# Kernel optimization log

Hardware: AMD Instinct MI355X
Metric: run time of the kernel (lower is better)

## Reference

```python
import jax, jax.numpy as jnp
import numpy as np

N_EMBED = 1024
HIDDEN = 2752  # find_multiple(int(8/3*1024), 32)
NUM_EXPERTS = 8
TOP_K = 2
AUX_COEFF = 0.01


def _swiglu(x, wg, wu, wd):
    # x: [N,C]; wg,wu: [H,C]; wd: [C,H]  (nn.Linear weight layout, y = x @ W.T)
    return (jax.nn.silu(x @ wg.T) * (x @ wu.T)) @ wd.T


def setup_inputs() -> dict:
    key = jax.random.key(0)
    ks = jax.random.split(key, 8)
    s = 0.02
    return {
        "x": jax.random.normal(ks[0], (2, 2048, N_EMBED), dtype=jnp.float32),
        "gate_w": jax.random.normal(ks[1], (NUM_EXPERTS, N_EMBED), dtype=jnp.float32) * s,
        "expert_gate_w": jax.random.normal(ks[2], (NUM_EXPERTS, HIDDEN, N_EMBED), dtype=jnp.float32) * s,
        "expert_up_w": jax.random.normal(ks[3], (NUM_EXPERTS, HIDDEN, N_EMBED), dtype=jnp.float32) * s,
        "expert_down_w": jax.random.normal(ks[4], (NUM_EXPERTS, N_EMBED, HIDDEN), dtype=jnp.float32) * s,
        "shared_gate_w": jax.random.normal(ks[5], (HIDDEN, N_EMBED), dtype=jnp.float32) * s,
        "shared_up_w": jax.random.normal(ks[6], (HIDDEN, N_EMBED), dtype=jnp.float32) * s,
        "shared_down_w": jax.random.normal(ks[7], (N_EMBED, HIDDEN), dtype=jnp.float32) * s,
    }


def reference(x, gate_w, expert_gate_w, expert_up_w, expert_down_w,
              shared_gate_w, shared_up_w, shared_down_w):
    B, T, C = x.shape
    xf = x.reshape(-1, C)                      # [N, C]
    N = xf.shape[0]

    # shared expert (always-on)
    shared_out = _swiglu(xf, shared_gate_w, shared_up_w, shared_down_w)

    # gating
    logits = xf @ gate_w.T                     # [N, E]
    top_w, top_i = jax.lax.top_k(logits, TOP_K)
    top_w = jax.nn.softmax(top_w.astype(jnp.float32), axis=-1)  # [N, K]

    # load-balancing aux loss
    mask = jax.nn.one_hot(top_i, NUM_EXPERTS, dtype=jnp.float32).sum(axis=1)  # [N, E]
    frac_selected = mask.mean(axis=0)
    mean_probs = jax.nn.softmax(logits.astype(jnp.float32), axis=-1).mean(axis=0)
    aux_loss = AUX_COEFF * (frac_selected * mean_probs).sum()

    # dense per-token per-expert combine weights (0 for unselected experts)
    w_dense = jnp.zeros((N, NUM_EXPERTS), jnp.float32)
    w_dense = w_dense.at[jnp.arange(N)[:, None], top_i].add(top_w)  # [N, E]

    routed = jnp.zeros_like(xf)
    for e in range(NUM_EXPERTS):
        routed = routed + _swiglu(xf, expert_gate_w[e], expert_up_w[e],
                                  expert_down_w[e]) * w_dense[:, e:e + 1]

    final = (shared_out + routed).reshape(B, T, C)
    return final, aux_loss
```

## Files before the change

### kernel.cpp

```cpp
#include <hip/hip_runtime.h>
#include <hip/hip_bf16.h>
#include <math.h>

#define N_TOK 4096
#define CDIM 1024
#define HDIM 2752
#define NEXP 8

typedef __bf16 bf16_t;
typedef __bf16 bf16x8 __attribute__((ext_vector_type(8)));
typedef float f32x4 __attribute__((ext_vector_type(4)));

__device__ __forceinline__ void gload_lds16(const void* g, void* l) {
  __builtin_amdgcn_global_load_lds(
      (const __attribute__((address_space(1))) unsigned int*)g,
      (__attribute__((address_space(3))) unsigned int*)l, 16, 0, 0);
}

__device__ __forceinline__ int xcd_swz(int orig, int nwg) {
  int q = nwg >> 3, r = nwg & 7;
  int xcd = orig & 7, lin = orig >> 3;
  return (xcd < r ? xcd * (q + 1) : r * (q + 1) + (xcd - r) * q) + lin;
}

struct CastG {
  const float* src[4];
  bf16_t* dst[4];
  int start[5];
  const float* x;
  const float* gw;
  int* top_i; float* top_w; float* probs_tok; bf16_t* xb;
};
__global__ void moe_cast_gate(CastG c) {
  const int b = blockIdx.x;
  if (b < c.start[4]) {
    int k = 0;
#pragma unroll
    for (int i = 0; i < 3; ++i) k += (b >= c.start[i + 1]);
    size_t i4 = (size_t)(b - c.start[k]) * 256 + threadIdx.x;
    float4 v = ((const float4*)c.src[k])[i4];
    union { bf16_t b4[4]; unsigned long long u; } pk;
    pk.b4[0] = (bf16_t)v.x; pk.b4[1] = (bf16_t)v.y;
    pk.b4[2] = (bf16_t)v.z; pk.b4[3] = (bf16_t)v.w;
    ((unsigned long long*)c.dst[k])[i4] = pk.u;
    return;
  }
  const int gb = b - c.start[4];
  const int wid = threadIdx.x >> 6, lane = threadIdx.x & 63;
  const int n = gb * 4 + wid;
  const float* xr = c.x + (size_t)n * CDIM;
  float xv[16];
  for (int j = 0; j < 16; j += 4)
    *(float4*)&xv[j] = *(const float4*)(xr + lane * 16 + j);
  {
    union { bf16_t bb[4]; unsigned long long u; } pk;
    unsigned long long* dst = (unsigned long long*)(c.xb + (size_t)n * CDIM + lane * 16);
    for (int j = 0; j < 16; j += 4) {
      pk.bb[0] = (bf16_t)xv[j]; pk.bb[1] = (bf16_t)xv[j+1];
      pk.bb[2] = (bf16_t)xv[j+2]; pk.bb[3] = (bf16_t)xv[j+3];
      dst[j >> 2] = pk.u;
    }
  }
  double part[NEXP];
  for (int e = 0; e < NEXP; ++e) {
    const float* gr = c.gw + e * CDIM + lane * 16;
    double s = 0.0;
    for (int j = 0; j < 16; j += 4) {
      float4 g = *(const float4*)(gr + j);
      s += (double)xv[j] * g.x + (double)xv[j+1] * g.y + (double)xv[j+2] * g.z + (double)xv[j+3] * g.w;
    }
    part[e] = s;
  }
  for (int off = 32; off; off >>= 1)
    for (int e = 0; e < NEXP; ++e) part[e] += __shfl_xor(part[e], off);
  if (lane == 0) {
    int i0 = 0; double l0 = part[0];
    for (int e = 1; e < NEXP; ++e) if (part[e] > l0) { l0 = part[e]; i0 = e; }
    int i1 = -1; double l1 = -1e300;
    for (int e = 0; e < NEXP; ++e) if (e != i0 && part[e] > l1) { l1 = part[e]; i1 = e; }
    double ed = exp(l1 - l0);
    float w0 = (float)(1.0 / (1.0 + ed));
    float w1 = (float)(ed / (1.0 + ed));
    c.top_i[2*n] = i0; c.top_i[2*n+1] = i1;
    c.top_w[2*n] = w0; c.top_w[2*n+1] = w1;
    double Z = 0.0, pe[NEXP];
    for (int e = 0; e < NEXP; ++e) { pe[e] = exp(part[e] - l0); Z += pe[e]; }
    for (int e = 0; e < NEXP; ++e) c.probs_tok[(size_t)n * NEXP + e] = (float)(pe[e] / Z);
  }
}

__global__ __launch_bounds__(256) void moe_reduce16(
    const float* __restrict__ probs_tok, const int* __restrict__ top_i,
    int* __restrict__ pcnt, float* __restrict__ psum) {
  const int b = blockIdx.x, t = threadIdx.x;
  const int wid = t >> 6, lane = t & 63;
  const int n = b * 256 + t;
  const int e0 = top_i[2*n], e1 = top_i[2*n + 1];
  float4 p0 = ((const float4*)(probs_tok + (size_t)n * NEXP))[0];
  float4 p1 = ((const float4*)(probs_tok + (size_t)n * NEXP))[1];
  float pv[8] = {p0.x, p0.y, p0.z, p0.w, p1.x, p1.y, p1.z, p1.w};
  __shared__ int lc[4][NEXP];
  __shared__ float ls[4][NEXP];
  for (int e = 0; e < NEXP; ++e) {
    int c = (e0 == e) + (e1 == e);
    float s = pv[e];
    for (int o = 32; o; o >>= 1) { c += __shfl_xor(c, o); s += __shfl_xor(s, o); }
    if (lane == 0) { lc[wid][e] = c; ls[wid][e] = s; }
  }
  __syncthreads();
  if (t < NEXP) {
    pcnt[b * NEXP + t] = lc[0][t] + lc[1][t] + lc[2][t] + lc[3][t];
    psum[b * NEXP + t] = ls[0][t] + ls[1][t] + ls[2][t] + ls[3][t];
  }
}

__global__ __launch_bounds__(256) void moe_scatter16(
    const int* __restrict__ top_i, const float* __restrict__ top_w,
    const int* __restrict__ pcnt, const float* __restrict__ psum,
    int* __restrict__ cnts_g, int* __restrict__ offs_g,
    int* __restrict__ rowlist, float* __restrict__ wlist,
    int* __restrict__ pair_pos, float* __restrict__ out_aux) {
  const int b = blockIdx.x, t = threadIdx.x;
  const int wid = t >> 6, lane = t & 63;
  __shared__ int tot_s[NEXP], pre_s[NEXP], offs_s[NEXP];
  __shared__ int wc[4][NEXP];
  if (t < NEXP) {
    int e = t, tot = 0, pre = 0;
    for (int bb = 0; bb < 16; ++bb) {
      int v = pcnt[bb * NEXP + e];
      pre += (bb < b) ? v : 0;
      tot += v;
    }
    tot_s[e] = tot; pre_s[e] = pre;
  }
  __syncthreads();
  if (t == 0) {
    int o = 0;
    for (int e = 0; e < NEXP; ++e) { offs_s[e] = o; o += tot_s[e]; }
    if (b == 0) {
      double aux = 0.0;
      for (int e = 0; e < NEXP; ++e) {
        float ps = 0.f;
        for (int bb = 0; bb < 16; ++bb) ps += psum[bb * NEXP + e];
        aux += (double)tot_s[e] * (double)ps;
        cnts_g[e] = tot_s[e]; offs_g[e] = offs_s[e];
      }
      out_aux[0] = (float)(0.01 * aux / ((double)N_TOK * (double)N_TOK));
    }
  }
  __syncthreads();
  const int n = b * 256 + t;
  const int e0 = top_i[2*n], e1 = top_i[2*n + 1];
  const float w0 = top_w[2*n], w1 = top_w[2*n + 1];
  for (int e = 0; e < NEXP; ++e) {
    unsigned long long m0 = __ballot(e0 == e);
    unsigned long long m1 = __ballot(e1 == e);
    if (lane == 0) wc[wid][e] = __popcll(m0) + __popcll(m1);
  }
  __syncthreads();
  const unsigned long long lt = ((unsigned long long)1 << lane) - 1;
  for (int e = 0; e < NEXP; ++e) {
    unsigned long long m0 = __ballot(e0 == e);
    unsigned long long m1 = __ballot(e1 == e);
    int wp = 0;
    for (int w = 0; w < wid; ++w) wp += wc[w][e];
    int base = offs_s[e] + pre_s[e] + wp;
    if (e0 == e) {
      int p = base + __popcll(m0 & lt);
      rowlist[p] = n; wlist[p] = w0; pair_pos[2*n] = p;
    }
    if (e1 == e) {
      int p = base + __popcll(m0) + __popcll(m1 & lt);
      rowlist[p] = n; wlist[p] = w1; pair_pos[2*n + 1] = p;
    }
  }
}

__launch_bounds__(256)
__global__ void moe_gu(const bf16_t* __restrict__ xb,
                       const bf16_t* __restrict__ Wg_r, const bf16_t* __restrict__ Wu_r,
                       const bf16_t* __restrict__ Wg_s, const bf16_t* __restrict__ Wu_s,
                       bf16_t* __restrict__ hout,
                       const int* __restrict__ rowlist, const int* __restrict__ offs,
                       const int* __restrict__ cnts,
                       const float* __restrict__ edw_f, const float* __restrict__ sdw_f,
                       bf16_t* __restrict__ edw_b, bf16_t* __restrict__ sdw_b) {
  const int z = blockIdx.z;
  if (z == NEXP + 1) {
    const int lb = blockIdx.x + (HDIM / 64) * blockIdx.y;
    const size_t E4 = (size_t)NEXP * HDIM * CDIM / 4;
    const size_t S4 = (size_t)HDIM * CDIM / 4;
    const size_t tot4 = E4 + S4;
    const size_t stride = (size_t)(HDIM / 64) * (N_TOK / 128) * 256;
    for (size_t i4 = (size_t)lb * 256 + threadIdx.x; i4 < tot4; i4 += stride) {
      float4 v; unsigned long long* d;
      if (i4 < E4) { v = ((const float4*)edw_f)[i4]; d = (unsigned long long*)edw_b + i4; }
      else { size_t j = i4 - E4; v = ((const float4*)sdw_f)[j]; d = (unsigned long long*)sdw_b + j; }
      union { bf16_t b4[4]; unsigned long long u; } pk;
      pk.b4[0] = (bf16_t)v.x; pk.b4[1] = (bf16_t)v.y;
      pk.b4[2] = (bf16_t)v.z; pk.b4[3] = (bf16_t)v.w;
      *d = pk.u;
    }
    return;
  }
  const bool routed = z < NEXP;
  int cnt, hbase, loff = 0;
  const bf16_t *Wg, *Wu;
  if (routed) {
    cnt = cnts[z]; loff = offs[z]; hbase = loff;
    if ((int)blockIdx.y * 128 >= cnt) return;
    Wg = Wg_r + (size_t)z * HDIM * CDIM;
    Wu = Wu_r + (size_t)z * HDIM * CDIM;
  } else {
    cnt = N_TOK; hbase = 2 * N_TOK;
    Wg = Wg_s; Wu = Wu_s;
  }
  const int m0 = blockIdx.y * 128, n0 = blockIdx.x * 64;

  __shared__ alignas(16) bf16_t lA[128 * 64];
  __shared__ alignas(16) bf16_t lB[128 * 64];

  const int tid = threadIdx.x, wid = tid >> 6, lane = tid & 63;
  const int r8 = lane >> 3, c8 = lane & 7;
  const int fr = lane & 15, hi = lane >> 4;

  const bf16_t* gA[4];
  for (int i = 0; i < 4; ++i) {
    int r = wid * 32 + i * 8 + r8;
    int tok;
    if (routed) { int mm = m0 + r < cnt ? m0 + r : cnt - 1; tok = rowlist[loff + mm]; }
    else tok = m0 + r;
    gA[i] = xb + (size_t)tok * CDIM + c8 * 8;
  }
  const bf16_t* gB[4];
  for (int i = 0; i < 4; ++i) {
    int br = wid * 32 + i * 8 + r8;
    gB[i] = (br < 64 ? Wg + (size_t)(n0 + br) * CDIM
                     : Wu + (size_t)(n0 + br - 64) * CDIM) + c8 * 8;
  }

  f32x4 accG[2][4] = {}; f32x4 accU[2][4] = {};

  for (int kt = 0; kt < CDIM / 64; ++kt) {
    if (kt) __syncthreads();
    for (int i = 0; i < 4; ++i) gload_lds16(gA[i] + kt * 64, lA + (wid * 32 + i * 8) * 64);
    for (int i = 0; i < 4; ++i) gload_lds16(gB[i] + kt * 64, lB + (wid * 32 + i * 8) * 64);
    __syncthreads();
    for (int kk = 0; kk < 2; ++kk) {
      const int kb = kk * 32 + hi * 8;
      bf16x8 a[2], bg[4], bu[4];
      for (int i = 0; i < 2; ++i) a[i] = *(const bf16x8*)(lA + (wid * 32 + i * 16 + fr) * 64 + kb);
      for (int j = 0; j < 4; ++j) {
        bg[j] = *(const bf16x8*)(lB + (j * 16 + fr) * 64 + kb);
        bu[j] = *(const bf16x8*)(lB + (64 + j * 16 + fr) * 64 + kb);
      }
      for (int i = 0; i < 2; ++i)
        for (int j = 0; j < 4; ++j) {
          accG[i][j] = __builtin_amdgcn_mfma_f32_16x16x32_bf16(a[i], bg[j], accG[i][j], 0, 0, 0);
          accU[i][j] = __builtin_amdgcn_mfma_f32_16x16x32_bf16(a[i], bu[j], accU[i][j], 0, 0, 0);
        }
    }
  }
  {
    bf16_t* myb = lA + wid * 32 * 64;
    for (int i = 0; i < 2; ++i)
      for (int j = 0; j < 4; ++j)
        for (int r = 0; r < 4; ++r) {
          int lrow = i * 16 + hi * 4 + r;
          float g = accG[i][j][r], u = accU[i][j][r];
          float hv = (g / (1.f + __expf(-g))) * u;
          myb[lrow * 64 + j * 16 + fr] = (bf16_t)hv;
        }
    asm volatile("s_waitcnt lgkmcnt(0)" ::: "memory");
    __builtin_amdgcn_sched_barrier(0);
    for (int round = 0; round < 4; ++round) {
      int lrow = round * 8 + (lane >> 3);
      int grow = m0 + wid * 32 + lrow;
      if (routed && grow >= cnt) continue;
      bf16x8 v = *(const bf16x8*)(myb + lrow * 64 + (lane & 7) * 8);
      *(bf16x8*)(hout + (size_t)(hbase + grow) * HDIM + n0 + (lane & 7) * 8) = v;
    }
  }
}

__launch_bounds__(256)
__global__ void moe_down(const bf16_t* __restrict__ hin, const bf16_t* __restrict__ Wd_r,
                         const bf16_t* __restrict__ Wd_s,
                         float* __restrict__ outp, float* __restrict__ eo,
                         const float* __restrict__ wlist,
                         const int* __restrict__ offs, const int* __restrict__ cnts) {
  const int z = blockIdx.z;
  const bool routed = z < NEXP;
  const int wg = xcd_swz(blockIdx.x, (CDIM / 128) * (N_TOK / 128));
  const int ym = wg & 31, xn = wg >> 5;
  int cnt, hbase;
  const bf16_t* Wd;
  if (routed) {
    cnt = cnts[z]; hbase = offs[z];
    if (ym * 128 >= cnt) return;
    Wd = Wd_r + (size_t)z * CDIM * HDIM;
  } else {
    cnt = N_TOK; hbase = 2 * N_TOK;
    Wd = Wd_s;
  }
  const int m0 = ym * 128, n0 = xn * 128;

  __shared__ alignas(16) bf16_t lA[128 * 64];
  __shared__ alignas(16) bf16_t lB[128 * 64];

  const int tid = threadIdx.x, wid = tid >> 6, lane = tid & 63;
  const int wm = wid >> 1, wn = wid & 1;
  const int r8 = lane >> 3, c8 = lane & 7;
  const int fr = lane & 15, hi = lane >> 4;

  const bf16_t* gA[4];
  for (int i = 0; i < 4; ++i) {
    int r = wid * 32 + i * 8 + r8;
    int mm = (routed && m0 + r >= cnt) ? cnt - 1 : m0 + r;
    gA[i] = hin + (size_t)(hbase + mm) * HDIM + c8 * 8;
  }
  const bf16_t* gB[4];
  for (int i = 0; i < 4; ++i) {
    int br = wid * 32 + i * 8 + r8;
    gB[i] = Wd + (size_t)(n0 + br) * HDIM + c8 * 8;
  }

  f32x4 acc[4][4] = {};

  for (int kt = 0; kt < HDIM / 64; ++kt) {
    if (kt) __syncthreads();
    for (int i = 0; i < 4; ++i) gload_lds16(gA[i] + kt * 64, lA + (wid * 32 + i * 8) * 64);
    for (int i = 0; i < 4; ++i) gload_lds16(gB[i] + kt * 64, lB + (wid * 32 + i * 8) * 64);
    __syncthreads();
    for (int kk = 0; kk < 2; ++kk) {
      const int kb = kk * 32 + hi * 8;
      bf16x8 a[4], b[4];
      for (int i = 0; i < 4; ++i) a[i] = *(const bf16x8*)(lA + (wm * 64 + i * 16 + fr) * 64 + kb);
      for (int j = 0; j < 4; ++j) b[j] = *(const bf16x8*)(lB + (wn * 64 + j * 16 + fr) * 64 + kb);
      for (int i = 0; i < 4; ++i)
        for (int j = 0; j < 4; ++j)
          acc[i][j] = __builtin_amdgcn_mfma_f32_16x16x32_bf16(a[i], b[j], acc[i][j], 0, 0, 0);
    }
  }
  for (int i = 0; i < 4; ++i)
    for (int j = 0; j < 4; ++j)
      for (int r = 0; r < 4; ++r) {
        int lm = wm * 64 + i * 16 + hi * 4 + r;
        if (routed && m0 + lm >= cnt) continue;
        float v = acc[i][j][r];
        int col = n0 + wn * 64 + j * 16 + fr;
        if (routed) {
          int pos = hbase + m0 + lm;
          eo[(size_t)pos * CDIM + col] = v * wlist[pos];
        } else {
          outp[(size_t)(m0 + lm) * CDIM + col] = v;
        }
      }
}

__global__ void moe_combine(float* __restrict__ outp, const float* __restrict__ eo,
                            const int* __restrict__ pair_pos) {
  size_t i4 = (size_t)blockIdx.x * 256 + threadIdx.x;
  int n = (int)(i4 >> 8);
  int c4 = (int)(i4 & 255);
  int p0 = pair_pos[2*n], p1 = pair_pos[2*n + 1];
  const float4* eo4 = (const float4*)eo;
  float4 a = ((const float4*)outp)[i4];
  float4 b = eo4[(size_t)p0 * 256 + c4];
  float4 c = eo4[(size_t)p1 * 256 + c4];
  float4 r;
  r.x = a.x + b.x + c.x; r.y = a.y + b.y + c.y;
  r.z = a.z + b.z + c.z; r.w = a.w + b.w + c.w;
  ((float4*)outp)[i4] = r;
}

extern "C" void kernel_launch(void* const* d_in, const int* in_sizes, int n_in,
                              void* d_out, int out_size, void* d_ws, size_t ws_size,
                              hipStream_t stream) {
  const float* x   = (const float*)d_in[0];
  const float* gw  = (const float*)d_in[1];
  const float* egw = (const float*)d_in[2];
  const float* euw = (const float*)d_in[3];
  const float* edw = (const float*)d_in[4];
  const float* sgw = (const float*)d_in[5];
  const float* suw = (const float*)d_in[6];
  const float* sdw = (const float*)d_in[7];
  float* out = (float*)d_out;

  char* ws = (char*)d_ws;
  size_t off = 0;
  auto alloc = [&](size_t bytes) -> void* {
    void* p = ws + off; off = (off + bytes + 255) & ~(size_t)255; return p;
  };
  const size_t EW = (size_t)NEXP * HDIM * CDIM;
  const size_t SW = (size_t)HDIM * CDIM;
  bf16_t* xb    = (bf16_t*)alloc((size_t)N_TOK * CDIM * 2);
  bf16_t* egw_b = (bf16_t*)alloc(EW * 2);
  bf16_t* euw_b = (bf16_t*)alloc(EW * 2);
  bf16_t* edw_b = (bf16_t*)alloc(EW * 2);
  bf16_t* sgw_b = (bf16_t*)alloc(SW * 2);
  bf16_t* suw_b = (bf16_t*)alloc(SW * 2);
  bf16_t* sdw_b = (bf16_t*)alloc(SW * 2);
  bf16_t* h     = (bf16_t*)alloc((size_t)(3 * N_TOK + 256) * HDIM * 2);
  float*  eo    = (float*)alloc((size_t)2 * N_TOK * CDIM * 4);
  int*    ctrl  = (int*)alloc(256);
  int* cnts = ctrl; int* offs = ctrl + 8;
  int*   top_i    = (int*)alloc((size_t)N_TOK * 2 * 4);
  float* top_w    = (float*)alloc((size_t)N_TOK * 2 * 4);
  int*   pair_pos = (int*)alloc((size_t)N_TOK * 2 * 4);
  int*   rowlist  = (int*)alloc((size_t)2 * N_TOK * 4);
  float* wlist    = (float*)alloc((size_t)2 * N_TOK * 4);
  float* probs_tok = (float*)alloc((size_t)N_TOK * NEXP * 4);
  int*   pcnt     = (int*)alloc(16 * NEXP * 4);
  float* psum     = (float*)alloc(16 * NEXP * 4);

  CastG cg;
  cg.src[0] = egw; cg.dst[0] = egw_b;
  cg.src[1] = euw; cg.dst[1] = euw_b;
  cg.src[2] = sgw; cg.dst[2] = sgw_b;
  cg.src[3] = suw; cg.dst[3] = suw_b;
  int ew_blk = (int)(EW / 1024), sw_blk = (int)(SW / 1024);
  cg.start[0] = 0;
  cg.start[1] = ew_blk;
  cg.start[2] = 2 * ew_blk;
  cg.start[3] = 2 * ew_blk + sw_blk;
  cg.start[4] = 2 * ew_blk + 2 * sw_blk;
  cg.x = x; cg.gw = gw;
  cg.top_i = top_i; cg.top_w = top_w; cg.probs_tok = probs_tok; cg.xb = xb;
  moe_cast_gate<<<cg.start[4] + N_TOK / 4, 256, 0, stream>>>(cg);

  moe_reduce16<<<16, 256, 0, stream>>>(probs_tok, top_i, pcnt, psum);
  moe_scatter16<<<16, 256, 0, stream>>>(top_i, top_w, pcnt, psum, cnts, offs,
                                        rowlist, wlist, pair_pos,
                                        out + (size_t)N_TOK * CDIM);

  moe_gu<<<dim3(HDIM / 64, N_TOK / 128, NEXP + 2), 256, 0, stream>>>(
      xb, egw_b, euw_b, sgw_b, suw_b, h, rowlist, offs, cnts,
      edw, sdw, edw_b, sdw_b);
  moe_down<<<dim3((CDIM / 128) * (N_TOK / 128), 1, NEXP + 1), 256, 0, stream>>>(
      h, edw_b, sdw_b, out, eo, wlist, offs, cnts);
  moe_combine<<<4096, 256, 0, stream>>>(out, eo, pair_pos);
}
```

Baseline: 474.9 us.

## Store routed expert outputs in bf16 and dispatch down-weight cast first

Routed expert partial outputs are now written as bf16 instead of fp32, which halves the traffic to write them in moe_down and to read them back in moe_combine. The combine kernel now handles 8 elements per thread and launches half as many blocks. In moe_gu the fp32-to-bf16 cast of the down weights moves from the last z-slice to z=0 so it is dispatched first. The bf16 intermediate adds rounding error to the routed contribution before it is summed.

Result: no change. 476.8 us (+0.4%).

```diff
diff --git a/kernel.cpp b/kernel.cpp
--- a/kernel.cpp
+++ b/kernel.cpp
@@ -186,7 +186,7 @@
                        const float* __restrict__ edw_f, const float* __restrict__ sdw_f,
                        bf16_t* __restrict__ edw_b, bf16_t* __restrict__ sdw_b) {
   const int z = blockIdx.z;
-  if (z == NEXP + 1) {
+  if (z == 0) {
     const int lb = blockIdx.x + (HDIM / 64) * blockIdx.y;
     const size_t E4 = (size_t)NEXP * HDIM * CDIM / 4;
     const size_t S4 = (size_t)HDIM * CDIM / 4;
@@ -203,14 +203,15 @@
     }
     return;
   }
-  const bool routed = z < NEXP;
+  const bool routed = z <= NEXP;
+  const int e = z - 1;
   int cnt, hbase, loff = 0;
   const bf16_t *Wg, *Wu;
   if (routed) {
-    cnt = cnts[z]; loff = offs[z]; hbase = loff;
+    cnt = cnts[e]; loff = offs[e]; hbase = loff;
     if ((int)blockIdx.y * 128 >= cnt) return;
-    Wg = Wg_r + (size_t)z * HDIM * CDIM;
-    Wu = Wu_r + (size_t)z * HDIM * CDIM;
+    Wg = Wg_r + (size_t)e * HDIM * CDIM;
+    Wu = Wu_r + (size_t)e * HDIM * CDIM;
   } else {
     cnt = N_TOK; hbase = 2 * N_TOK;
     Wg = Wg_s; Wu = Wu_s;
@@ -286,7 +287,7 @@
 __launch_bounds__(256)
 __global__ void moe_down(const bf16_t* __restrict__ hin, const bf16_t* __restrict__ Wd_r,
                          const bf16_t* __restrict__ Wd_s,
-                         float* __restrict__ outp, float* __restrict__ eo,
+                         float* __restrict__ outp, bf16_t* __restrict__ eo,
                          const float* __restrict__ wlist,
                          const int* __restrict__ offs, const int* __restrict__ cnts) {
   const int z = blockIdx.z;
@@ -351,27 +352,30 @@
         int col = n0 + wn * 64 + j * 16 + fr;
         if (routed) {
           int pos = hbase + m0 + lm;
-          eo[(size_t)pos * CDIM + col] = v * wlist[pos];
+          eo[(size_t)pos * CDIM + col] = (bf16_t)(v * wlist[pos]);
         } else {
           outp[(size_t)(m0 + lm) * CDIM + col] = v;
         }
       }
 }
 
-__global__ void moe_combine(float* __restrict__ outp, const float* __restrict__ eo,
+__global__ void moe_combine(float* __restrict__ outp, const bf16_t* __restrict__ eo,
                             const int* __restrict__ pair_pos) {
-  size_t i4 = (size_t)blockIdx.x * 256 + threadIdx.x;
-  int n = (int)(i4 >> 8);
-  int c4 = (int)(i4 & 255);
+  size_t i8 = (size_t)blockIdx.x * 256 + threadIdx.x;
+  int n = (int)(i8 >> 7);
+  int c8 = (int)(i8 & 127) * 8;
   int p0 = pair_pos[2*n], p1 = pair_pos[2*n + 1];
-  const float4* eo4 = (const float4*)eo;
-  float4 a = ((const float4*)outp)[i4];
-  float4 b = eo4[(size_t)p0 * 256 + c4];
-  float4 c = eo4[(size_t)p1 * 256 + c4];
-  float4 r;
-  r.x = a.x + b.x + c.x; r.y = a.y + b.y + c.y;
-  r.z = a.z + b.z + c.z; r.w = a.w + b.w + c.w;
-  ((float4*)outp)[i4] = r;
+  bf16x8 b0 = *(const bf16x8*)(eo + (size_t)p0 * CDIM + c8);
+  bf16x8 b1 = *(const bf16x8*)(eo + (size_t)p1 * CDIM + c8);
+  float* op = outp + (size_t)n * CDIM + c8;
+  float4 a0 = *(float4*)op;
+  float4 a1 = *(float4*)(op + 4);
+  a0.x += (float)b0[0] + (float)b1[0]; a0.y += (float)b0[1] + (float)b1[1];
+  a0.z += (float)b0[2] + (float)b1[2]; a0.w += (float)b0[3] + (float)b1[3];
+  a1.x += (float)b0[4] + (float)b1[4]; a1.y += (float)b0[5] + (float)b1[5];
+  a1.z += (float)b0[6] + (float)b1[6]; a1.w += (float)b0[7] + (float)b1[7];
+  *(float4*)op = a0;
+  *(float4*)(op + 4) = a1;
 }
 
 extern "C" void kernel_launch(void* const* d_in, const int* in_sizes, int n_in,
@@ -402,7 +406,7 @@
   bf16_t* suw_b = (bf16_t*)alloc(SW * 2);
   bf16_t* sdw_b = (bf16_t*)alloc(SW * 2);
   bf16_t* h     = (bf16_t*)alloc((size_t)(3 * N_TOK + 256) * HDIM * 2);
-  float*  eo    = (float*)alloc((size_t)2 * N_TOK * CDIM * 4);
+  bf16_t* eo    = (bf16_t*)alloc((size_t)2 * N_TOK * CDIM * 2);
   int*    ctrl  = (int*)alloc(256);
   int* cnts = ctrl; int* offs = ctrl + 8;
   int*   top_i    = (int*)alloc((size_t)N_TOK * 2 * 4);
@@ -439,5 +443,5 @@
       edw, sdw, edw_b, sdw_b);
   moe_down<<<dim3((CDIM / 128) * (N_TOK / 128), 1, NEXP + 1), 256, 0, stream>>>(
       h, edw_b, sdw_b, out, eo, wlist, offs, cnts);
-  moe_combine<<<4096, 256, 0, stream>>>(out, eo, pair_pos);
-}
+  moe_combine<<<2048, 256, 0, stream>>>(out, eo, pair_pos);
+}
```
